# Kernel tuning notes

Hardware: AMD Instinct MI355X
Metric: run time of the kernel (lower is better)

## Reference

```python
import jax, jax.numpy as jnp
import numpy as np

C = 256; CM = 8; MAXI = 100; NCLS = 80
KP = (CM + 2) * CM + CM + CM * CM + CM + CM + 1  # 169 dynamic-kernel params

def _ln(x, g, b, eps=1e-5):
    m = x.mean(-1, keepdims=True)
    v = ((x - m) ** 2).mean(-1, keepdims=True)
    return g * (x - m) * jax.lax.rsqrt(v + eps) + b

def _mlp(x, hw, hb, lng, lnb, fw, fb):
    # torchvision MLP: [Linear -> LayerNorm -> SiLU] * n_hidden -> Linear
    for i in range(hw.shape[0]):
        x = jax.nn.silu(_ln(x @ hw[i] + hb[i], lng[i], lnb[i]))
    return x @ fw + fb

def _conv1x1_bn(x, w, s, b):
    # 1x1 conv (no bias) + inference-mode BatchNorm folded into per-channel affine
    y = jnp.einsum('bchw,oc->bohw', x, w)
    return y * s[None, :, None, None] + b[None, :, None, None]

def _grid(h, w):
    # normalized cell-center coordinates, (x, y) order, shape [h, w, 2]
    ys = (jnp.arange(h, dtype=jnp.float32) + 0.5) / h
    xs = (jnp.arange(w, dtype=jnp.float32) + 0.5) / w
    return jnp.stack([jnp.broadcast_to(xs[None, :], (h, w)),
                      jnp.broadcast_to(ys[:, None], (h, w))], axis=-1)

def setup_inputs() -> dict:
    key = jax.random.key(0)
    ks = iter(jax.random.split(key, 40))
    nrm = lambda shape, s=0.02: s * jax.random.normal(next(ks), shape, jnp.float32)
    B = 4
    inp = {
        'x0': jax.random.normal(next(ks), (B, 3, 512, 512), jnp.float32),
        'x1': jax.random.normal(next(ks), (B, 64, 256, 256), jnp.float32),
        'x2': jax.random.normal(next(ks), (B, 128, 128, 128), jnp.float32),
        'x3': jax.random.normal(next(ks), (B, 256, 64, 64), jnp.float32),
        'x4': jax.random.normal(next(ks), (B, 512, 32, 32), jnp.float32),
        'x5': jax.random.normal(next(ks), (B, 1024, 16, 16), jnp.float32),
        'lat3_w': nrm((C, 256)), 'lat3_s': jnp.ones((C,)), 'lat3_b': jnp.zeros((C,)),
        'lat4_w': nrm((C, 512)), 'lat4_s': jnp.ones((C,)), 'lat4_b': jnp.zeros((C,)),
        'lat5_w': nrm((C, 1024)), 'lat5_s': jnp.ones((C,)), 'lat5_b': jnp.zeros((C,)),
        'mlat_w': nrm((C, 256)), 'mlat_s': jnp.ones((C,)), 'mlat_b': jnp.zeros((C,)),
        'mhead_w': nrm((CM, C, 3, 3)), 'mhead_s': jnp.ones((CM,)), 'mhead_b': jnp.zeros((CM,)),
        'loc_hw': nrm((4, C, C)), 'loc_hb': jnp.zeros((4, C)), 'loc_lng': jnp.ones((4, C)), 'loc_lnb': jnp.zeros((4, C)),
        'loc_fw': nrm((C, 1)), 'loc_fb': -5.0 * jnp.ones((1,)),
        'cls_hw': nrm((4, C, C)), 'cls_hb': jnp.zeros((4, C)), 'cls_lng': jnp.ones((4, C)), 'cls_lnb': jnp.zeros((4, C)),
        'cls_fw': nrm((C, NCLS)), 'cls_fb': jnp.zeros((NCLS,)),
        'ker_hw': nrm((4, C, C)), 'ker_hb': jnp.zeros((4, C)), 'ker_lng': jnp.ones((4, C)), 'ker_lnb': jnp.zeros((4, C)),
        'ker_fw': nrm((C, KP)), 'ker_fb': jnp.zeros((KP,)),
    }
    return inp

def reference(x0, x1, x2, x3, x4, x5,
              lat3_w, lat3_s, lat3_b, lat4_w, lat4_s, lat4_b, lat5_w, lat5_s, lat5_b,
              mlat_w, mlat_s, mlat_b, mhead_w, mhead_s, mhead_b,
              loc_hw, loc_hb, loc_lng, loc_lnb, loc_fw, loc_fb,
              cls_hw, cls_hb, cls_lng, cls_lnb, cls_fw, cls_fb,
              ker_hw, ker_hb, ker_lng, ker_lnb, ker_fw, ker_fb):
    B, _, H, W = x0.shape
    lvls = [(x3, lat3_w, lat3_s, lat3_b), (x4, lat4_w, lat4_s, lat4_b), (x5, lat5_w, lat5_s, lat5_b)]
    feats = [_conv1x1_bn(x, w, s, b) for (x, w, s, b) in lvls]
    flat = jnp.concatenate([f.reshape(B, C, -1).transpose(0, 2, 1) for f in feats], axis=1)  # [B, L, C]
    loc_logits = _mlp(flat, loc_hw, loc_hb, loc_lng, loc_lnb, loc_fw, loc_fb)[..., 0]       # [B, L]
    top_vals, top_idx = jax.lax.top_k(loc_logits, MAXI)
    scores = jax.nn.sigmoid(top_vals)
    num_instances = (scores > 0.5).sum(axis=1)
    gfeat = jnp.take_along_axis(flat, top_idx[:, :, None], axis=1)  # [B, I, C]
    # mask branch
    mf = _conv1x1_bn(x3, mlat_w, mlat_s, mlat_b)
    mf = jax.lax.conv_general_dilated(mf, mhead_w, (1, 1), 'SAME', dimension_numbers=('NCHW', 'OIHW', 'NCHW'))
    mf = jax.nn.silu(mf * mhead_s[None, :, None, None] + mhead_b[None, :, None, None])  # [B, CM, h3, w3]
    h3, w3 = x3.shape[2], x3.shape[3]
    offs_flat = jnp.concatenate([_grid(x.shape[2], x.shape[3]).reshape(-1, 2) for x in (x3, x4, x5)], axis=0)
    offs = offs_flat[top_idx]                                # [B, I, 2]
    grid = _grid(h3, w3).transpose(2, 0, 1)                  # [2, h3, w3]
    grid = grid[None, None] - offs[:, :, :, None, None]      # [B, I, 2, h, w]
    mfi = jnp.broadcast_to(mf[:, None], (B, MAXI, CM, h3, w3))
    feats_i = jnp.concatenate([mfi, grid], axis=2)           # [B, I, CM+2, h, w]
    dyn = _mlp(gfeat, ker_hw, ker_hb, ker_lng, ker_lnb, ker_fw, ker_fb)  # [B, I, KP]
    c = CM
    o = (c + 2) * c
    w1 = dyn[..., :o].reshape(B, MAXI, c + 2, c)
    b1 = dyn[..., o:o + c].reshape(B, MAXI, c, 1, 1); o += c
    w2 = dyn[..., o:o + c * c].reshape(B, MAXI, c, c); o += c * c
    b2 = dyn[..., o:o + c].reshape(B, MAXI, c, 1, 1); o += c
    w3 = dyn[..., o:o + c].reshape(B, MAXI, c, 1); o += c
    b3 = dyn[..., o:].reshape(B, MAXI, 1, 1, 1)
    m = jax.nn.silu(jnp.einsum('bichw,bicd->bidhw', feats_i, w1) + b1)
    m = jax.nn.silu(jnp.einsum('bichw,bicd->bidhw', m, w2) + b2)
    m = jnp.einsum('bichw,bicd->bidhw', m, w3) + b3
    masks = jax.nn.sigmoid(m[:, :, 0])                       # [B, I, h3, w3]
    classes = jnp.argmax(_mlp(gfeat, cls_hw, cls_hb, cls_lng, cls_lnb, cls_fw, cls_fb), axis=-1)
    masks = jax.image.resize(masks, (B, MAXI, H, W), method='bilinear', antialias=False)
    return (num_instances, scores, classes, masks)
```

## Files before the change

kernel.cpp:

```cpp
#include <hip/hip_runtime.h>
#include <hip/hip_bf16.h>
#include <math.h>

#define DEVI __device__ __forceinline__

constexpr int LTOT  = 5376;
constexpr int NINST = 100;
constexpr int NCLS  = 80;
constexpr int KPAR  = 169;

DEVI float waveAllSum(float v) {
#pragma unroll
  for (int s = 32; s > 0; s >>= 1) v += __shfl_xor(v, s, 64);
  return v;
}
DEVI float siluf(float x) { return x / (1.0f + expf(-x)); }
DEVI float sigmf(float x) { return 1.0f / (1.0f + expf(-x)); }

template<int MODE>
__global__ __launch_bounds__(256) void mlp_layer(
    const float* __restrict__ in, float* __restrict__ out,
    const float* __restrict__ w0, const float* __restrict__ hb0,
    const float* __restrict__ g0, const float* __restrict__ lb0,
    const float* __restrict__ w1, const float* __restrict__ hb1,
    const float* __restrict__ g1, const float* __restrict__ lb1,
    const float* __restrict__ fw, const float* __restrict__ fb,
    float* __restrict__ logits, int rowDelta)
{
  __shared__ float xs[256][20];
  __shared__ float wsm[32][256];
  const int tid = threadIdx.x;
  const int rg = tid >> 6, cg = tid & 63;
  const long r0 = (long)blockIdx.x * 16;
  bool set1 = false;
  const float *w = w0, *hb = hb0, *g = g0, *lb = lb0;
  if (MODE == 2) {
    set1 = (blockIdx.x >= (gridDim.x >> 1));
    if (set1) { w = w1; hb = hb1; g = g1; lb = lb1; }
  }
  const long ir0 = r0 + ((MODE == 2 && set1) ? rowDelta : 0);
  {
    const int i = tid >> 4, kq = tid & 15;
    const float4* src = reinterpret_cast<const float4*>(in + (ir0 + i) * 256);
#pragma unroll
    for (int qq = 0; qq < 4; ++qq) {
      const int k4 = kq + 16 * qq;
      const float4 v = src[k4];
      xs[4*k4+0][i] = v.x; xs[4*k4+1][i] = v.y;
      xs[4*k4+2][i] = v.z; xs[4*k4+3][i] = v.w;
    }
  }
  float acc[4][4] = {};
  for (int kb = 0; kb < 8; ++kb) {
    __syncthreads();
    {
      const float4* w4 = reinterpret_cast<const float4*>(w + kb*32*256);
#pragma unroll
      for (int qb = 0; qb < 8; ++qb) {
        const int c = tid + 256*qb;
        const float4 f = w4[c];
        *reinterpret_cast<float4*>(&wsm[c>>6][4*(c&63)]) = f;
      }
    }
    __syncthreads();
#pragma unroll
    for (int kk = 0; kk < 32; ++kk) {
      const float4 wv = *reinterpret_cast<const float4*>(&wsm[kk][4*cg]);
      const float4 av = *reinterpret_cast<const float4*>(&xs[kb*32+kk][4*rg]);
      const float ar[4] = {av.x, av.y, av.z, av.w};
#pragma unroll
      for (int i = 0; i < 4; ++i) {
        acc[i][0] += ar[i]*wv.x; acc[i][1] += ar[i]*wv.y;
        acc[i][2] += ar[i]*wv.z; acc[i][3] += ar[i]*wv.w;
      }
    }
  }
  const float4 hb4 = *reinterpret_cast<const float4*>(&hb[4*cg]);
  const float4 g4  = *reinterpret_cast<const float4*>(&g[4*cg]);
  const float4 lb4 = *reinterpret_cast<const float4*>(&lb[4*cg]);
  float4 fw4 = {0,0,0,0}; float fbv = 0.f;
  if (MODE == 1) { fw4 = *reinterpret_cast<const float4*>(&fw[4*cg]); fbv = fb[0]; }
#pragma unroll
  for (int i = 0; i < 4; ++i) {
    float y0 = acc[i][0]+hb4.x, y1 = acc[i][1]+hb4.y;
    float y2 = acc[i][2]+hb4.z, y3 = acc[i][3]+hb4.w;
    const float m = waveAllSum(y0+y1+y2+y3) * (1.0f/256.0f);
    const float d0=y0-m, d1=y1-m, d2=y2-m, d3=y3-m;
    const float var = waveAllSum(d0*d0+d1*d1+d2*d2+d3*d3) * (1.0f/256.0f);
    const float rs = rsqrtf(var + 1e-5f);
    const float4 ov = { siluf(g4.x*d0*rs + lb4.x), siluf(g4.y*d1*rs + lb4.y),
                        siluf(g4.z*d2*rs + lb4.z), siluf(g4.w*d3*rs + lb4.w) };
    if (MODE == 1) {
      float dot = ov.x*fw4.x + ov.y*fw4.y + ov.z*fw4.z + ov.w*fw4.w;
      dot = waveAllSum(dot);
      if (cg == 0) logits[r0 + 4*rg + i] = dot + fbv;
    } else {
      *reinterpret_cast<float4*>(&out[(r0 + 4*rg + i)*256 + 4*cg]) = ov;
    }
  }
}

__global__ __launch_bounds__(256) void lateral_all(
    const float* __restrict__ x3, const float* __restrict__ x4, const float* __restrict__ x5,
    const float* __restrict__ w3, const float* __restrict__ s3, const float* __restrict__ b3,
    const float* __restrict__ w4, const float* __restrict__ s4, const float* __restrict__ b4,
    const float* __restrict__ w5, const float* __restrict__ s5, const float* __restrict__ b5,
    const float* __restrict__ wm, const float* __restrict__ sm, const float* __restrict__ bm,
    float* __restrict__ flat, float* __restrict__ mlatb)
{
  __shared__ float xs[32][20];
  __shared__ float wsm[32][256];
  const int tid = threadIdx.x;
  const int rg = tid >> 6, cg = tid & 63;
  const int bid = blockIdx.x;
  const float *x, *w, *sc, *bi; int K, P, pshift, rel, baseL; bool trans = true;
  if (bid < 1024)      { rel=bid;      x=x3; w=w3; sc=s3; bi=b3; K=256;  P=4096; pshift=8; baseL=0; }
  else if (bid < 1280) { rel=bid-1024; x=x4; w=w4; sc=s4; bi=b4; K=512;  P=1024; pshift=6; baseL=4096; }
  else if (bid < 1344) { rel=bid-1280; x=x5; w=w5; sc=s5; bi=b5; K=1024; P=256;  pshift=4; baseL=5120; }
  else                 { rel=bid-1344; x=x3; w=wm; sc=sm; bi=bm; K=256;  P=4096; pshift=8; baseL=0; trans=false; }
  const int b = rel >> pshift;
  const int p0 = (rel - (b << pshift)) << 4;
  const float* xb = x + (long)b * K * P;
  float acc[4][4] = {};
  const int nkb = K >> 5;
  for (int kb = 0; kb < nkb; ++kb) {
    __syncthreads();
    {
      const int kk = tid >> 4, i = tid & 15;
      xs[kk][i]    = xb[(long)(kb*32 + kk)*P + p0 + i];
      xs[kk+16][i] = xb[(long)(kb*32 + kk + 16)*P + p0 + i];
    }
    {
      const float4* wr = reinterpret_cast<const float4*>(w + (long)tid*K + kb*32);
#pragma unroll
      for (int kq = 0; kq < 8; ++kq) {
        const float4 v = wr[kq];
        wsm[4*kq+0][tid]=v.x; wsm[4*kq+1][tid]=v.y;
        wsm[4*kq+2][tid]=v.z; wsm[4*kq+3][tid]=v.w;
      }
    }
    __syncthreads();
#pragma unroll
    for (int kk = 0; kk < 32; ++kk) {
      const float4 wv = *reinterpret_cast<const float4*>(&wsm[kk][4*cg]);
      const float4 av = *reinterpret_cast<const float4*>(&xs[kk][4*rg]);
      const float ar[4] = {av.x, av.y, av.z, av.w};
#pragma unroll
      for (int i = 0; i < 4; ++i) {
        acc[i][0]+=ar[i]*wv.x; acc[i][1]+=ar[i]*wv.y;
        acc[i][2]+=ar[i]*wv.z; acc[i][3]+=ar[i]*wv.w;
      }
    }
  }
  const float4 s4v = *reinterpret_cast<const float4*>(&sc[4*cg]);
  const float4 b4v = *reinterpret_cast<const float4*>(&bi[4*cg]);
  if (trans) {
#pragma unroll
    for (int i = 0; i < 4; ++i) {
      const float4 ov = { acc[i][0]*s4v.x+b4v.x, acc[i][1]*s4v.y+b4v.y,
                          acc[i][2]*s4v.z+b4v.z, acc[i][3]*s4v.w+b4v.w };
      *reinterpret_cast<float4*>(&flat[((long)b*LTOT + baseL + p0 + 4*rg + i)*256 + 4*cg]) = ov;
    }
  } else {
    const float ss[4] = {s4v.x, s4v.y, s4v.z, s4v.w};
    const float bb[4] = {b4v.x, b4v.y, b4v.z, b4v.w};
#pragma unroll
    for (int j = 0; j < 4; ++j) {
      const float4 ov = { acc[0][j]*ss[j]+bb[j], acc[1][j]*ss[j]+bb[j],
                          acc[2][j]*ss[j]+bb[j], acc[3][j]*ss[j]+bb[j] };
      *reinterpret_cast<float4*>(&mlatb[((long)b*256 + 4*cg + j)*(long)P + p0 + 4*rg]) = ov;
    }
  }
}

__global__ __launch_bounds__(256) void topk_gather(
    const float* __restrict__ logits, const float* __restrict__ flat,
    int* __restrict__ topi, float* __restrict__ gfeat,
    float* __restrict__ dout)
{
  __shared__ float sv[LTOT];
  __shared__ float rv[4];
  __shared__ int   ri[4];
  __shared__ int   sidx[NINST];
  const int b = blockIdx.x, tid = threadIdx.x;
  for (int l = tid; l < LTOT; l += 256) sv[l] = logits[b*LTOT + l];
  __syncthreads();
  int cnt = 0;
  for (int t = 0; t < NINST; ++t) {
    float bv = -INFINITY; int bidx = 0x7fffffff;
    for (int l = tid; l < LTOT; l += 256) {
      const float v = sv[l];
      if (v > bv) { bv = v; bidx = l; }
    }
#pragma unroll
    for (int s = 32; s > 0; s >>= 1) {
      const float v2 = __shfl_xor(bv, s, 64);
      const int   i2 = __shfl_xor(bidx, s, 64);
      if (v2 > bv || (v2 == bv && i2 < bidx)) { bv = v2; bidx = i2; }
    }
    if ((tid & 63) == 0) { rv[tid >> 6] = bv; ri[tid >> 6] = bidx; }
    __syncthreads();
    if (tid == 0) {
      bv = rv[0]; bidx = ri[0];
#pragma unroll
      for (int q = 1; q < 4; ++q)
        if (rv[q] > bv || (rv[q] == bv && ri[q] < bidx)) { bv = rv[q]; bidx = ri[q]; }
      sidx[t] = bidx; topi[b*NINST + t] = bidx;
      dout[4 + b*NINST + t] = sigmf(bv);
      if (bv > 0.0f) ++cnt;
      sv[bidx] = -INFINITY;
    }
    __syncthreads();
  }
  if (tid == 0) dout[b] = (float)cnt;
  for (int t = 0; t < NINST; ++t) {
    const int ix = sidx[t];
    gfeat[((long)b*NINST + t)*256 + tid] = flat[((long)b*LTOT + ix)*256 + tid];
  }
}

__global__ __launch_bounds__(256) void heads(
    const float* __restrict__ h2, const float* __restrict__ cfw, const float* __restrict__ cfb,
    const float* __restrict__ kfw, const float* __restrict__ kfb,
    float* __restrict__ dout, float* __restrict__ dyn)
{
  __shared__ float xr[256];
  __shared__ float lv[NCLS];
  const int bid = blockIdx.x, tid = threadIdx.x;
  xr[tid] = h2[(long)bid*256 + tid];
  __syncthreads();
  if (bid < 400) {
    if (tid < NCLS) {
      float a0=0.f, a1=0.f, a2=0.f, a3=0.f;
      for (int k = 0; k < 256; k += 4) {
        a0 += xr[k+0]*cfw[(k+0)*NCLS + tid];
        a1 += xr[k+1]*cfw[(k+1)*NCLS + tid];
        a2 += xr[k+2]*cfw[(k+2)*NCLS + tid];
        a3 += xr[k+3]*cfw[(k+3)*NCLS + tid];
      }
      lv[tid] = (a0+a1) + (a2+a3) + cfb[tid];
    }
    __syncthreads();
    if (tid == 0) {
      float bv = lv[0]; int bi2 = 0;
      for (int o = 1; o < NCLS; ++o) if (lv[o] > bv) { bv = lv[o]; bi2 = o; }
      dout[404 + bid] = (float)bi2;
    }
  } else {
    if (tid < KPAR) {
      float a0=0.f, a1=0.f, a2=0.f, a3=0.f;
      for (int k = 0; k < 256; k += 4) {
        a0 += xr[k+0]*kfw[(k+0)*KPAR + tid];
        a1 += xr[k+1]*kfw[(k+1)*KPAR + tid];
        a2 += xr[k+2]*kfw[(k+2)*KPAR + tid];
        a3 += xr[k+3]*kfw[(k+3)*KPAR + tid];
      }
      dyn[(long)(bid-400)*KPAR + tid] = (a0+a1) + (a2+a3) + kfb[tid];
    }
  }
}

__global__ __launch_bounds__(256) void conv3(
    const float* __restrict__ mlat, const float* __restrict__ mw,
    float* __restrict__ partial)
{
  const int bid = blockIdx.x;
  const int cc = bid & 7;
  const int tile = (bid >> 3) & 15;
  const int b = bid >> 7;
  const int y0 = (tile >> 2)*16, x0 = (tile & 3)*16;
  const int tid = threadIdx.x;
  const int ly = tid >> 4, lx = tid & 15;
  __shared__ float til[2][18][19];
  __shared__ float wch[8][32][12];
  for (int e = tid; e < 2304; e += 256) {
    const int o = e / 288, rem = e % 288;
    const int c = rem / 9, qq = rem - c*9;
    wch[o][c][qq] = mw[((o*256) + cc*32 + c)*9 + qq];
  }
  int lofs[3], gofs[3], chn[3]; bool vld[3], has[3];
  float* tf = &til[0][0][0];
#pragma unroll
  for (int s = 0; s < 3; ++s) {
    const int e = tid + 256*s;
    has[s] = (e < 648);
    lofs[s] = 0; gofs[s] = 0; chn[s] = 0; vld[s] = false;
    if (has[s]) {
      const int ch = (e >= 324) ? 1 : 0;
      const int pos = e - ch*324;
      const int iy = pos / 18, ix = pos - iy*18;
      const int gy = y0 - 1 + iy, gx = x0 - 1 + ix;
      vld[s] = (gy >= 0 && gy < 64 && gx >= 0 && gx < 64);
      lofs[s] = ch*342 + iy*19 + ix;
      gofs[s] = gy*64 + gx;
      chn[s] = ch;
    }
  }
  const float* xbase = mlat + ((long)b*256 + cc*32)*4096;
  float acc[8] = {};
  for (int r = 0; r < 16; ++r) {
    __syncthreads();
#pragma unroll
    for (int s = 0; s < 3; ++s)
      if (has[s]) tf[lofs[s]] = vld[s] ? xbase[(long)(2*r + chn[s])*4096 + gofs[s]] : 0.f;
    __syncthreads();
#pragma unroll
    for (int ch = 0; ch < 2; ++ch) {
      const int c = 2*r + ch;
      float t[9];
#pragma unroll
      for (int dy = 0; dy < 3; ++dy)
#pragma unroll
        for (int dx = 0; dx < 3; ++dx) t[dy*3+dx] = til[ch][ly+dy][lx+dx];
#pragma unroll
      for (int o = 0; o < 8; ++o) {
        const float4 wa = *reinterpret_cast<const float4*>(&wch[o][c][0]);
        const float4 wb = *reinterpret_cast<const float4*>(&wch[o][c][4]);
        const float w8 = wch[o][c][8];
        acc[o] += t[0]*wa.x + t[1]*wa.y + t[2]*wa.z + t[3]*wa.w
                + t[4]*wb.x + t[5]*wb.y + t[6]*wb.z + t[7]*wb.w + t[8]*w8;
      }
    }
  }
  const long pbase = (((long)b*8 + cc)*8)*4096 + (y0+ly)*64 + (x0+lx);
#pragma unroll
  for (int o = 0; o < 8; ++o) partial[pbase + (long)o*4096] = acc[o];
}

__global__ __launch_bounds__(256) void mhead_fin(
    const float* __restrict__ partial, const float* __restrict__ s,
    const float* __restrict__ bi, float* __restrict__ mhead)
{
  const int idx = blockIdx.x*256 + threadIdx.x;
  const int p = idx & 4095;
  const int o = (idx >> 12) & 7;
  const int b = idx >> 15;
  float v = 0.f;
#pragma unroll
  for (int cc = 0; cc < 8; ++cc) v += partial[(((long)b*8 + cc)*8 + o)*4096 + p];
  v = v*s[o] + bi[o];
  mhead[idx] = siluf(v);
}

__global__ __launch_bounds__(256) void mask_fused(
    const float* __restrict__ dyn, const int* __restrict__ topi,
    const float* __restrict__ mhead, float* __restrict__ dout)
{
  __shared__ float msrc[18][64];
  __shared__ float dd[KPAR];
  __shared__ float so[2];
  const int bid = blockIdx.x;
  const int inst = bid >> 2, q = bid & 3;
  const int tid = threadIdx.x;
  if (tid < KPAR) dd[tid] = dyn[(long)inst*KPAR + tid];
  if (tid == 0) {
    const int l = topi[inst];
    float ox, oy;
    if (l < 4096)      { ox = ((l & 63) + 0.5f)*(1.f/64.f); oy = ((l >> 6) + 0.5f)*(1.f/64.f); }
    else if (l < 5120) { const int t = l - 4096; ox = ((t & 31) + 0.5f)*(1.f/32.f); oy = ((t >> 5) + 0.5f)*(1.f/32.f); }
    else               { const int t = l - 5120; ox = ((t & 15) + 0.5f)*(1.f/16.f); oy = ((t >> 4) + 0.5f)*(1.f/16.f); }
    so[0] = ox; so[1] = oy;
  }
  __syncthreads();
  const float ox = so[0], oy = so[1];
  const int b = inst / NINST;
  const float* mh = mhead + (long)b*8*4096;
  const int r0s = 16*q - 1;
  for (int e = tid; e < 1152; e += 256) {
    const int r = e >> 6, x = e & 63;
    int sy = r0s + r; sy = sy < 0 ? 0 : (sy > 63 ? 63 : sy);
    const int p = sy*64 + x;
    float f[10];
#pragma unroll
    for (int c = 0; c < 8; ++c) f[c] = mh[c*4096 + p];
    f[8] = (x + 0.5f)*(1.f/64.f) - ox;
    f[9] = (sy + 0.5f)*(1.f/64.f) - oy;
    float m1[8];
#pragma unroll
    for (int d = 0; d < 8; ++d) {
      float t = dd[80 + d];
#pragma unroll
      for (int c = 0; c < 10; ++c) t += f[c]*dd[c*8 + d];
      m1[d] = siluf(t);
    }
    float m2[8];
#pragma unroll
    for (int d = 0; d < 8; ++d) {
      float t = dd[152 + d];
#pragma unroll
      for (int c = 0; c < 8; ++c) t += m1[c]*dd[88 + c*8 + d];
      m2[d] = siluf(t);
    }
    float o = dd[168];
#pragma unroll
    for (int c = 0; c < 8; ++c) o += m2[c]*dd[160 + c];
    msrc[r][x] = sigmf(o);
  }
  __syncthreads();
  const int j4 = tid & 127;
  const int half = tid >> 7;
  const int ix0 = (j4 & 1) ? (j4 >> 1) : (j4 >> 1) - 1;
  const int xlo = ix0 < 0 ? 0 : ix0;
  const int xhi = (ix0 + 1 > 63) ? 63 : ix0 + 1;
  float fx[4];
#pragma unroll
  for (int m = 0; m < 4; ++m) {
    const int x = 4*j4 + m;
    const float tx = (x + 0.5f)*0.125f - 0.5f;
    fx[m] = tx - (float)ix0;
  }
  float* dbase = dout + 804 + ((long)inst << 18);
  for (int it = 0; it < 64; ++it) {
    const int yy = 2*it + half;
    const int y = 128*q + yy;
    const float ty = (y + 0.5f)*0.125f - 0.5f;
    const float fyf = floorf(ty);
    const int iy0 = (int)fyf;
    const float fy = ty - fyf;
    const int r0 = iy0 - r0s;
    const float L0 = msrc[r0][xlo],   R0 = msrc[r0][xhi];
    const float L1 = msrc[r0+1][xlo], R1 = msrc[r0+1][xhi];
    const float L = L0 + (L1 - L0)*fy;
    const float R = R0 + (R1 - R0)*fy;
    const float4 ov = { L + (R - L)*fx[0], L + (R - L)*fx[1],
                        L + (R - L)*fx[2], L + (R - L)*fx[3] };
    *reinterpret_cast<float4*>(&dbase[((long)y << 9) + (j4 << 2)]) = ov;
  }
}

extern "C" void kernel_launch(void* const* d_in, const int* in_sizes, int n_in,
                              void* d_out, int out_size, void* d_ws, size_t ws_size,
                              hipStream_t stream)
{
  (void)in_sizes; (void)n_in; (void)out_size; (void)ws_size;
  const float* x3      = (const float*)d_in[3];
  const float* x4      = (const float*)d_in[4];
  const float* x5      = (const float*)d_in[5];
  const float* lat3_w  = (const float*)d_in[6];
  const float* lat3_s  = (const float*)d_in[7];
  const float* lat3_b  = (const float*)d_in[8];
  const float* lat4_w  = (const float*)d_in[9];
  const float* lat4_s  = (const float*)d_in[10];
  const float* lat4_b  = (const float*)d_in[11];
  const float* lat5_w  = (const float*)d_in[12];
  const float* lat5_s  = (const float*)d_in[13];
  const float* lat5_b  = (const float*)d_in[14];
  const float* mlat_w  = (const float*)d_in[15];
  const float* mlat_s  = (const float*)d_in[16];
  const float* mlat_b  = (const float*)d_in[17];
  const float* mhead_w = (const float*)d_in[18];
  const float* mhead_s = (const float*)d_in[19];
  const float* mhead_b = (const float*)d_in[20];
  const float* loc_hw  = (const float*)d_in[21];
  const float* loc_hb  = (const float*)d_in[22];
  const float* loc_lng = (const float*)d_in[23];
  const float* loc_lnb = (const float*)d_in[24];
  const float* loc_fw  = (const float*)d_in[25];
  const float* loc_fb  = (const float*)d_in[26];
  const float* cls_hw  = (const float*)d_in[27];
  const float* cls_hb  = (const float*)d_in[28];
  const float* cls_lng = (const float*)d_in[29];
  const float* cls_lnb = (const float*)d_in[30];
  const float* cls_fw  = (const float*)d_in[31];
  const float* cls_fb  = (const float*)d_in[32];
  const float* ker_hw  = (const float*)d_in[33];
  const float* ker_hb  = (const float*)d_in[34];
  const float* ker_lng = (const float*)d_in[35];
  const float* ker_lnb = (const float*)d_in[36];
  const float* ker_fw  = (const float*)d_in[37];
  const float* ker_fb  = (const float*)d_in[38];

  float* ws      = (float*)d_ws;
  float* flat    = ws;
  float* buf     = ws + 5505024;
  float* mlatb   = ws + 11010048;
  float* partial = ws + 15204352;
  float* mheadb  = ws + 16252928;
  float* h2      = ws + 16384000;
  float* logits  = ws + 16588800;
  int*   topi    = (int*)(ws + 16610304);
  float* gfeat   = ws + 16610704;
  float* dynb    = ws + 16713104;
  float* dout    = (float*)d_out;

  lateral_all<<<2368, 256, 0, stream>>>(x3, x4, x5,
      lat3_w, lat3_s, lat3_b, lat4_w, lat4_s, lat4_b, lat5_w, lat5_s, lat5_b,
      mlat_w, mlat_s, mlat_b, flat, mlatb);
  conv3<<<512, 256, 0, stream>>>(mlatb, mhead_w, partial);
  mhead_fin<<<512, 256, 0, stream>>>(partial, mhead_s, mhead_b, mheadb);
  mlp_layer<0><<<1344, 256, 0, stream>>>(flat, buf,
      loc_hw, loc_hb, loc_lng, loc_lnb, nullptr, nullptr, nullptr, nullptr,
      nullptr, nullptr, nullptr, 0);
  for (int i = 1; i < 3; ++i)
    mlp_layer<0><<<1344, 256, 0, stream>>>(buf, buf,
        loc_hw + i*65536, loc_hb + i*256, loc_lng + i*256, loc_lnb + i*256,
        nullptr, nullptr, nullptr, nullptr, nullptr, nullptr, nullptr, 0);
  mlp_layer<1><<<1344, 256, 0, stream>>>(buf, nullptr,
      loc_hw + 3*65536, loc_hb + 3*256, loc_lng + 3*256, loc_lnb + 3*256,
      nullptr, nullptr, nullptr, nullptr, loc_fw, loc_fb, logits, 0);
  topk_gather<<<4, 256, 0, stream>>>(logits, flat, topi, gfeat, dout);
  mlp_layer<2><<<50, 256, 0, stream>>>(gfeat, h2,
      cls_hw, cls_hb, cls_lng, cls_lnb, ker_hw, ker_hb, ker_lng, ker_lnb,
      nullptr, nullptr, nullptr, -400);
  for (int i = 1; i < 4; ++i)
    mlp_layer<2><<<50, 256, 0, stream>>>(h2, h2,
        cls_hw + i*65536, cls_hb + i*256, cls_lng + i*256, cls_lnb + i*256,
        ker_hw + i*65536, ker_hb + i*256, ker_lng + i*256, ker_lnb + i*256,
        nullptr, nullptr, nullptr, 0);
  heads<<<800, 256, 0, stream>>>(h2, cls_fw, cls_fb, ker_fw, ker_fb, dout, dynb);
  mask_fused<<<1600, 256, 0, stream>>>(dynb, topi, mheadb, dout);
}
```

Before: 864.1 us.

## Fuse MLP layers into single kernels and merge lateral/mask-lateral GEMMs

```diff
diff --git a/kernel.cpp b/kernel.cpp
--- a/kernel.cpp
+++ b/kernel.cpp
@@ -16,89 +16,6 @@
 }
 DEVI float siluf(float x) { return x / (1.0f + expf(-x)); }
 DEVI float sigmf(float x) { return 1.0f / (1.0f + expf(-x)); }
-
-template<int MODE>
-__global__ __launch_bounds__(256) void mlp_layer(
-    const float* __restrict__ in, float* __restrict__ out,
-    const float* __restrict__ w0, const float* __restrict__ hb0,
-    const float* __restrict__ g0, const float* __restrict__ lb0,
-    const float* __restrict__ w1, const float* __restrict__ hb1,
-    const float* __restrict__ g1, const float* __restrict__ lb1,
-    const float* __restrict__ fw, const float* __restrict__ fb,
-    float* __restrict__ logits, int rowDelta)
-{
-  __shared__ float xs[256][20];
-  __shared__ float wsm[32][256];
-  const int tid = threadIdx.x;
-  const int rg = tid >> 6, cg = tid & 63;
-  const long r0 = (long)blockIdx.x * 16;
-  bool set1 = false;
-  const float *w = w0, *hb = hb0, *g = g0, *lb = lb0;
-  if (MODE == 2) {
-    set1 = (blockIdx.x >= (gridDim.x >> 1));
-    if (set1) { w = w1; hb = hb1; g = g1; lb = lb1; }
-  }
-  const long ir0 = r0 + ((MODE == 2 && set1) ? rowDelta : 0);
-  {
-    const int i = tid >> 4, kq = tid & 15;
-    const float4* src = reinterpret_cast<const float4*>(in + (ir0 + i) * 256);
-#pragma unroll
-    for (int qq = 0; qq < 4; ++qq) {
-      const int k4 = kq + 16 * qq;
-      const float4 v = src[k4];
-      xs[4*k4+0][i] = v.x; xs[4*k4+1][i] = v.y;
-      xs[4*k4+2][i] = v.z; xs[4*k4+3][i] = v.w;
-    }
-  }
-  float acc[4][4] = {};
-  for (int kb = 0; kb < 8; ++kb) {
-    __syncthreads();
-    {
-      const float4* w4 = reinterpret_cast<const float4*>(w + kb*32*256);
-#pragma unroll
-      for (int qb = 0; qb < 8; ++qb) {
-        const int c = tid + 256*qb;
-        const float4 f = w4[c];
-        *reinterpret_cast<float4*>(&wsm[c>>6][4*(c&63)]) = f;
-      }
-    }
-    __syncthreads();
-#pragma unroll
-    for (int kk = 0; kk < 32; ++kk) {
-      const float4 wv = *reinterpret_cast<const float4*>(&wsm[kk][4*cg]);
-      const float4 av = *reinterpret_cast<const float4*>(&xs[kb*32+kk][4*rg]);
-      const float ar[4] = {av.x, av.y, av.z, av.w};
-#pragma unroll
-      for (int i = 0; i < 4; ++i) {
-        acc[i][0] += ar[i]*wv.x; acc[i][1] += ar[i]*wv.y;
-        acc[i][2] += ar[i]*wv.z; acc[i][3] += ar[i]*wv.w;
-      }
-    }
-  }
-  const float4 hb4 = *reinterpret_cast<const float4*>(&hb[4*cg]);
-  const float4 g4  = *reinterpret_cast<const float4*>(&g[4*cg]);
-  const float4 lb4 = *reinterpret_cast<const float4*>(&lb[4*cg]);
-  float4 fw4 = {0,0,0,0}; float fbv = 0.f;
-  if (MODE == 1) { fw4 = *reinterpret_cast<const float4*>(&fw[4*cg]); fbv = fb[0]; }
-#pragma unroll
-  for (int i = 0; i < 4; ++i) {
-    float y0 = acc[i][0]+hb4.x, y1 = acc[i][1]+hb4.y;
-    float y2 = acc[i][2]+hb4.z, y3 = acc[i][3]+hb4.w;
-    const float m = waveAllSum(y0+y1+y2+y3) * (1.0f/256.0f);
-    const float d0=y0-m, d1=y1-m, d2=y2-m, d3=y3-m;
-    const float var = waveAllSum(d0*d0+d1*d1+d2*d2+d3*d3) * (1.0f/256.0f);
-    const float rs = rsqrtf(var + 1e-5f);
-    const float4 ov = { siluf(g4.x*d0*rs + lb4.x), siluf(g4.y*d1*rs + lb4.y),
-                        siluf(g4.z*d2*rs + lb4.z), siluf(g4.w*d3*rs + lb4.w) };
-    if (MODE == 1) {
-      float dot = ov.x*fw4.x + ov.y*fw4.y + ov.z*fw4.z + ov.w*fw4.w;
-      dot = waveAllSum(dot);
-      if (cg == 0) logits[r0 + 4*rg + i] = dot + fbv;
-    } else {
-      *reinterpret_cast<float4*>(&out[(r0 + 4*rg + i)*256 + 4*cg]) = ov;
-    }
-  }
-}
 
 __global__ __launch_bounds__(256) void lateral_all(
     const float* __restrict__ x3, const float* __restrict__ x4, const float* __restrict__ x5,
@@ -108,68 +25,175 @@
     const float* __restrict__ wm, const float* __restrict__ sm, const float* __restrict__ bm,
     float* __restrict__ flat, float* __restrict__ mlatb)
 {
-  __shared__ float xs[32][20];
-  __shared__ float wsm[32][256];
+  __shared__ float xs[16][36];
+  __shared__ float wsA[16][256];
+  __shared__ float wsB[16][256];
   const int tid = threadIdx.x;
   const int rg = tid >> 6, cg = tid & 63;
   const int bid = blockIdx.x;
-  const float *x, *w, *sc, *bi; int K, P, pshift, rel, baseL; bool trans = true;
-  if (bid < 1024)      { rel=bid;      x=x3; w=w3; sc=s3; bi=b3; K=256;  P=4096; pshift=8; baseL=0; }
-  else if (bid < 1280) { rel=bid-1024; x=x4; w=w4; sc=s4; bi=b4; K=512;  P=1024; pshift=6; baseL=4096; }
-  else if (bid < 1344) { rel=bid-1280; x=x5; w=w5; sc=s5; bi=b5; K=1024; P=256;  pshift=4; baseL=5120; }
-  else                 { rel=bid-1344; x=x3; w=wm; sc=sm; bi=bm; K=256;  P=4096; pshift=8; baseL=0; trans=false; }
-  const int b = rel >> pshift;
-  const int p0 = (rel - (b << pshift)) << 4;
+  const float *x, *wA, *wB = nullptr, *scA, *biA;
+  int K, P, b, p0, baseL; bool merged = false;
+  if (bid < 512)      { merged = true; b = bid >> 7; p0 = (bid & 127) * 32;
+                        x = x3; wA = w3; wB = wm; scA = s3; biA = b3; K = 256; P = 4096; baseL = 0; }
+  else if (bid < 640) { const int rel = bid - 512; b = rel >> 5; p0 = (rel & 31) * 32;
+                        x = x4; wA = w4; scA = s4; biA = b4; K = 512; P = 1024; baseL = 4096; }
+  else                { const int rel = bid - 640; b = rel >> 3; p0 = (rel & 7) * 32;
+                        x = x5; wA = w5; scA = s5; biA = b5; K = 1024; P = 256; baseL = 5120; }
   const float* xb = x + (long)b * K * P;
-  float acc[4][4] = {};
-  const int nkb = K >> 5;
+  float accA[8][4] = {};
+  float accB[8][4] = {};
+  const int nkb = K >> 4;
   for (int kb = 0; kb < nkb; ++kb) {
     __syncthreads();
+#pragma unroll
+    for (int s = 0; s < 2; ++s) {
+      const int e = tid + 256*s;
+      const int kk = e >> 5, px = e & 31;
+      xs[kk][px] = xb[(kb*16 + kk)*P + p0 + px];
+    }
     {
-      const int kk = tid >> 4, i = tid & 15;
-      xs[kk][i]    = xb[(long)(kb*32 + kk)*P + p0 + i];
-      xs[kk+16][i] = xb[(long)(kb*32 + kk + 16)*P + p0 + i];
-    }
-    {
-      const float4* wr = reinterpret_cast<const float4*>(w + (long)tid*K + kb*32);
-#pragma unroll
-      for (int kq = 0; kq < 8; ++kq) {
-        const float4 v = wr[kq];
-        wsm[4*kq+0][tid]=v.x; wsm[4*kq+1][tid]=v.y;
-        wsm[4*kq+2][tid]=v.z; wsm[4*kq+3][tid]=v.w;
-      }
-    }
-    __syncthreads();
-#pragma unroll
-    for (int kk = 0; kk < 32; ++kk) {
-      const float4 wv = *reinterpret_cast<const float4*>(&wsm[kk][4*cg]);
-      const float4 av = *reinterpret_cast<const float4*>(&xs[kk][4*rg]);
-      const float ar[4] = {av.x, av.y, av.z, av.w};
-#pragma unroll
-      for (int i = 0; i < 4; ++i) {
-        acc[i][0]+=ar[i]*wv.x; acc[i][1]+=ar[i]*wv.y;
-        acc[i][2]+=ar[i]*wv.z; acc[i][3]+=ar[i]*wv.w;
-      }
-    }
-  }
-  const float4 s4v = *reinterpret_cast<const float4*>(&sc[4*cg]);
-  const float4 b4v = *reinterpret_cast<const float4*>(&bi[4*cg]);
-  if (trans) {
-#pragma unroll
-    for (int i = 0; i < 4; ++i) {
-      const float4 ov = { acc[i][0]*s4v.x+b4v.x, acc[i][1]*s4v.y+b4v.y,
-                          acc[i][2]*s4v.z+b4v.z, acc[i][3]*s4v.w+b4v.w };
-      *reinterpret_cast<float4*>(&flat[((long)b*LTOT + baseL + p0 + 4*rg + i)*256 + 4*cg]) = ov;
-    }
-  } else {
-    const float ss[4] = {s4v.x, s4v.y, s4v.z, s4v.w};
-    const float bb[4] = {b4v.x, b4v.y, b4v.z, b4v.w};
+      const float4* wr = reinterpret_cast<const float4*>(wA + (long)tid*K + kb*16);
+#pragma unroll
+      for (int q = 0; q < 4; ++q) {
+        const float4 v = wr[q];
+        wsA[4*q+0][tid]=v.x; wsA[4*q+1][tid]=v.y; wsA[4*q+2][tid]=v.z; wsA[4*q+3][tid]=v.w;
+      }
+      if (merged) {
+        const float4* wr2 = reinterpret_cast<const float4*>(wB + (long)tid*K + kb*16);
+#pragma unroll
+        for (int q = 0; q < 4; ++q) {
+          const float4 v = wr2[q];
+          wsB[4*q+0][tid]=v.x; wsB[4*q+1][tid]=v.y; wsB[4*q+2][tid]=v.z; wsB[4*q+3][tid]=v.w;
+        }
+      }
+    }
+    __syncthreads();
+#pragma unroll
+    for (int kk = 0; kk < 16; ++kk) {
+      const float4 a0 = *reinterpret_cast<const float4*>(&xs[kk][8*rg]);
+      const float4 a1 = *reinterpret_cast<const float4*>(&xs[kk][8*rg+4]);
+      const float ar[8] = {a0.x,a0.y,a0.z,a0.w,a1.x,a1.y,a1.z,a1.w};
+      const float4 wv = *reinterpret_cast<const float4*>(&wsA[kk][4*cg]);
+#pragma unroll
+      for (int i = 0; i < 8; ++i) {
+        accA[i][0] += ar[i]*wv.x; accA[i][1] += ar[i]*wv.y;
+        accA[i][2] += ar[i]*wv.z; accA[i][3] += ar[i]*wv.w;
+      }
+      if (merged) {
+        const float4 wv2 = *reinterpret_cast<const float4*>(&wsB[kk][4*cg]);
+#pragma unroll
+        for (int i = 0; i < 8; ++i) {
+          accB[i][0] += ar[i]*wv2.x; accB[i][1] += ar[i]*wv2.y;
+          accB[i][2] += ar[i]*wv2.z; accB[i][3] += ar[i]*wv2.w;
+        }
+      }
+    }
+  }
+  const float4 sA = *reinterpret_cast<const float4*>(&scA[4*cg]);
+  const float4 bA = *reinterpret_cast<const float4*>(&biA[4*cg]);
+#pragma unroll
+  for (int i = 0; i < 8; ++i) {
+    const float4 ov = { accA[i][0]*sA.x+bA.x, accA[i][1]*sA.y+bA.y,
+                        accA[i][2]*sA.z+bA.z, accA[i][3]*sA.w+bA.w };
+    *reinterpret_cast<float4*>(&flat[((long)b*LTOT + baseL + p0 + 8*rg + i)*256 + 4*cg]) = ov;
+  }
+  if (merged) {
+    const float4 sB = *reinterpret_cast<const float4*>(&sm[4*cg]);
+    const float4 bB = *reinterpret_cast<const float4*>(&bm[4*cg]);
 #pragma unroll
     for (int j = 0; j < 4; ++j) {
-      const float4 ov = { acc[0][j]*ss[j]+bb[j], acc[1][j]*ss[j]+bb[j],
-                          acc[2][j]*ss[j]+bb[j], acc[3][j]*ss[j]+bb[j] };
-      *reinterpret_cast<float4*>(&mlatb[((long)b*256 + 4*cg + j)*(long)P + p0 + 4*rg]) = ov;
-    }
+      const float sj = (&sB.x)[j], bj = (&bB.x)[j];
+      const float4 o0 = { accB[0][j]*sj+bj, accB[1][j]*sj+bj, accB[2][j]*sj+bj, accB[3][j]*sj+bj };
+      const float4 o1 = { accB[4][j]*sj+bj, accB[5][j]*sj+bj, accB[6][j]*sj+bj, accB[7][j]*sj+bj };
+      float* mb = &mlatb[((long)b*256 + 4*cg + j)*4096 + p0 + 8*rg];
+      *reinterpret_cast<float4*>(mb) = o0;
+      *reinterpret_cast<float4*>(mb + 4) = o1;
+    }
+  }
+}
+
+__global__ __launch_bounds__(256) void loc4(
+    const float* __restrict__ in, const float* __restrict__ hw,
+    const float* __restrict__ hb, const float* __restrict__ lng, const float* __restrict__ lnb,
+    const float* __restrict__ fw, const float* __restrict__ fb, float* __restrict__ logits)
+{
+  __shared__ float xs[256][36];
+  __shared__ float wsm[16][256];
+  const int tid = threadIdx.x;
+  const int rg = tid >> 6, cg = tid & 63;
+  const long r0 = (long)blockIdx.x * 32;
+#pragma unroll
+  for (int s = 0; s < 8; ++s) {
+    const int e = tid + 256*s;
+    const int row = e >> 6, q = e & 63;
+    const float4 v = *reinterpret_cast<const float4*>(&in[(r0 + row)*256 + 4*q]);
+    const int pc = 8*((row >> 3) ^ (q & 3)) + (row & 7);
+#pragma unroll
+    for (int j = 0; j < 4; ++j) xs[4*q+j][pc] = (&v.x)[j];
+  }
+  float ov[8][4];
+  for (int L = 0; L < 4; ++L) {
+    const float* w = hw + L*65536;
+    float acc[8][4] = {};
+    for (int kb = 0; kb < 16; ++kb) {
+      __syncthreads();
+      const float4* w4 = reinterpret_cast<const float4*>(w + (kb << 12));
+#pragma unroll
+      for (int q = 0; q < 4; ++q) {
+        const int c = tid + (q << 8);
+        *reinterpret_cast<float4*>(&wsm[c>>6][4*(c&63)]) = w4[c];
+      }
+      __syncthreads();
+#pragma unroll
+      for (int kk = 0; kk < 16; ++kk) {
+        const int k = (kb << 4) + kk;
+        const int col = 8*(rg ^ ((k >> 2) & 3));
+        const float4 a0 = *reinterpret_cast<const float4*>(&xs[k][col]);
+        const float4 a1 = *reinterpret_cast<const float4*>(&xs[k][col+4]);
+        const float4 wv = *reinterpret_cast<const float4*>(&wsm[kk][4*cg]);
+        const float ar[8] = {a0.x,a0.y,a0.z,a0.w,a1.x,a1.y,a1.z,a1.w};
+#pragma unroll
+        for (int i = 0; i < 8; ++i) {
+          acc[i][0] += ar[i]*wv.x; acc[i][1] += ar[i]*wv.y;
+          acc[i][2] += ar[i]*wv.z; acc[i][3] += ar[i]*wv.w;
+        }
+      }
+    }
+    const float4 hb4 = *reinterpret_cast<const float4*>(&hb[L*256 + 4*cg]);
+    const float4 g4  = *reinterpret_cast<const float4*>(&lng[L*256 + 4*cg]);
+    const float4 lb4 = *reinterpret_cast<const float4*>(&lnb[L*256 + 4*cg]);
+#pragma unroll
+    for (int i = 0; i < 8; ++i) {
+      const float y0 = acc[i][0]+hb4.x, y1 = acc[i][1]+hb4.y;
+      const float y2 = acc[i][2]+hb4.z, y3 = acc[i][3]+hb4.w;
+      const float m = waveAllSum(y0+y1+y2+y3) * (1.0f/256.0f);
+      const float d0=y0-m, d1=y1-m, d2=y2-m, d3=y3-m;
+      const float var = waveAllSum(d0*d0+d1*d1+d2*d2+d3*d3) * (1.0f/256.0f);
+      const float rs = rsqrtf(var + 1e-5f);
+      ov[i][0] = siluf(g4.x*d0*rs + lb4.x);
+      ov[i][1] = siluf(g4.y*d1*rs + lb4.y);
+      ov[i][2] = siluf(g4.z*d2*rs + lb4.z);
+      ov[i][3] = siluf(g4.w*d3*rs + lb4.w);
+    }
+    __syncthreads();
+    if (L < 3) {
+      const int colb = 8*(rg ^ (cg & 3));
+#pragma unroll
+      for (int j = 0; j < 4; ++j) {
+        const float4 t0 = {ov[0][j], ov[1][j], ov[2][j], ov[3][j]};
+        const float4 t1 = {ov[4][j], ov[5][j], ov[6][j], ov[7][j]};
+        *reinterpret_cast<float4*>(&xs[4*cg+j][colb])   = t0;
+        *reinterpret_cast<float4*>(&xs[4*cg+j][colb+4]) = t1;
+      }
+    }
+  }
+  const float4 fw4 = *reinterpret_cast<const float4*>(&fw[4*cg]);
+  const float fbv = fb[0];
+#pragma unroll
+  for (int i = 0; i < 8; ++i) {
+    float d = ov[i][0]*fw4.x + ov[i][1]*fw4.y + ov[i][2]*fw4.z + ov[i][3]*fw4.w;
+    d = waveAllSum(d);
+    if (cg == 0) logits[r0 + 8*rg + i] = d + fbv;
   }
 }
 
@@ -216,6 +240,88 @@
   for (int t = 0; t < NINST; ++t) {
     const int ix = sidx[t];
     gfeat[((long)b*NINST + t)*256 + tid] = flat[((long)b*LTOT + ix)*256 + tid];
+  }
+}
+
+__global__ __launch_bounds__(256) void clsker4(
+    const float* __restrict__ gfeat, float* __restrict__ h2,
+    const float* __restrict__ chw, const float* __restrict__ chb,
+    const float* __restrict__ cg_, const float* __restrict__ cb_,
+    const float* __restrict__ khw, const float* __restrict__ khb,
+    const float* __restrict__ kg_, const float* __restrict__ kb_)
+{
+  __shared__ float xs[256][12];
+  __shared__ float wsm[16][256];
+  const int tid = threadIdx.x;
+  const int rg = tid >> 6, cg = tid & 63;
+  const bool ker = blockIdx.x >= 50;
+  const int r0 = (ker ? (blockIdx.x - 50) : blockIdx.x) * 8;
+  const int outr0 = r0 + (ker ? 400 : 0);
+  const float* hw = ker ? khw : chw;
+  const float* hb = ker ? khb : chb;
+  const float* g_ = ker ? kg_ : cg_;
+  const float* lb = ker ? kb_ : cb_;
+#pragma unroll
+  for (int s = 0; s < 2; ++s) {
+    const int e = tid + 256*s;
+    const int row = e >> 6, q = e & 63;
+    const float4 v = *reinterpret_cast<const float4*>(&gfeat[(long)(r0 + row)*256 + 4*q]);
+    const int pc = 2*((row >> 1) ^ (q & 3)) + (row & 1);
+#pragma unroll
+    for (int j = 0; j < 4; ++j) xs[4*q+j][pc] = (&v.x)[j];
+  }
+  float ov[2][4];
+  for (int L = 0; L < 4; ++L) {
+    const float* w = hw + L*65536;
+    float acc[2][4] = {};
+    for (int kb = 0; kb < 16; ++kb) {
+      __syncthreads();
+      const float4* w4 = reinterpret_cast<const float4*>(w + (kb << 12));
+#pragma unroll
+      for (int q = 0; q < 4; ++q) {
+        const int c = tid + (q << 8);
+        *reinterpret_cast<float4*>(&wsm[c>>6][4*(c&63)]) = w4[c];
+      }
+      __syncthreads();
+#pragma unroll
+      for (int kk = 0; kk < 16; ++kk) {
+        const int k = (kb << 4) + kk;
+        const float2 av = *reinterpret_cast<const float2*>(&xs[k][2*(rg ^ ((k >> 2) & 3))]);
+        const float4 wv = *reinterpret_cast<const float4*>(&wsm[kk][4*cg]);
+        acc[0][0] += av.x*wv.x; acc[0][1] += av.x*wv.y; acc[0][2] += av.x*wv.z; acc[0][3] += av.x*wv.w;
+        acc[1][0] += av.y*wv.x; acc[1][1] += av.y*wv.y; acc[1][2] += av.y*wv.z; acc[1][3] += av.y*wv.w;
+      }
+    }
+    const float4 hb4 = *reinterpret_cast<const float4*>(&hb[L*256 + 4*cg]);
+    const float4 g4  = *reinterpret_cast<const float4*>(&g_[L*256 + 4*cg]);
+    const float4 lb4 = *reinterpret_cast<const float4*>(&lb[L*256 + 4*cg]);
+#pragma unroll
+    for (int i = 0; i < 2; ++i) {
+      const float y0 = acc[i][0]+hb4.x, y1 = acc[i][1]+hb4.y;
+      const float y2 = acc[i][2]+hb4.z, y3 = acc[i][3]+hb4.w;
+      const float m = waveAllSum(y0+y1+y2+y3) * (1.0f/256.0f);
+      const float d0=y0-m, d1=y1-m, d2=y2-m, d3=y3-m;
+      const float var = waveAllSum(d0*d0+d1*d1+d2*d2+d3*d3) * (1.0f/256.0f);
+      const float rs = rsqrtf(var + 1e-5f);
+      ov[i][0] = siluf(g4.x*d0*rs + lb4.x);
+      ov[i][1] = siluf(g4.y*d1*rs + lb4.y);
+      ov[i][2] = siluf(g4.z*d2*rs + lb4.z);
+      ov[i][3] = siluf(g4.w*d3*rs + lb4.w);
+    }
+    __syncthreads();
+    if (L < 3) {
+      const int pc = 2*(rg ^ (cg & 3));
+#pragma unroll
+      for (int j = 0; j < 4; ++j) {
+        const float2 t = {ov[0][j], ov[1][j]};
+        *reinterpret_cast<float2*>(&xs[4*cg+j][pc]) = t;
+      }
+    }
+  }
+#pragma unroll
+  for (int i = 0; i < 2; ++i) {
+    const float4 o = {ov[i][0], ov[i][1], ov[i][2], ov[i][3]};
+    *reinterpret_cast<float4*>(&h2[(long)(outr0 + 2*rg + i)*256 + 4*cg]) = o;
   }
 }
 
@@ -373,8 +479,8 @@
     float f[10];
 #pragma unroll
     for (int c = 0; c < 8; ++c) f[c] = mh[c*4096 + p];
-    f[8] = (x + 0.5f)*(1.f/64.f) - ox;
-    f[9] = (sy + 0.5f)*(1.f/64.f) - oy;
+    f[8] = ((x) + 0.5f)*(1.f/64.f) - ox;
+    f[9] = ((sy) + 0.5f)*(1.f/64.f) - oy;
     float m1[8];
 #pragma unroll
     for (int d = 0; d < 8; ++d) {
@@ -422,9 +528,9 @@
     const float L1 = msrc[r0+1][xlo], R1 = msrc[r0+1][xhi];
     const float L = L0 + (L1 - L0)*fy;
     const float R = R0 + (R1 - R0)*fy;
-    const float4 ov = { L + (R - L)*fx[0], L + (R - L)*fx[1],
-                        L + (R - L)*fx[2], L + (R - L)*fx[3] };
-    *reinterpret_cast<float4*>(&dbase[((long)y << 9) + (j4 << 2)]) = ov;
+    const float4 ovv = { L + (R - L)*fx[0], L + (R - L)*fx[1],
+                         L + (R - L)*fx[2], L + (R - L)*fx[3] };
+    *reinterpret_cast<float4*>(&dbase[((long)y << 9) + (j4 << 2)]) = ovv;
   }
 }
 
@@ -472,41 +578,26 @@
 
   float* ws      = (float*)d_ws;
   float* flat    = ws;
-  float* buf     = ws + 5505024;
-  float* mlatb   = ws + 11010048;
-  float* partial = ws + 15204352;
-  float* mheadb  = ws + 16252928;
-  float* h2      = ws + 16384000;
-  float* logits  = ws + 16588800;
-  int*   topi    = (int*)(ws + 16610304);
-  float* gfeat   = ws + 16610704;
-  float* dynb    = ws + 16713104;
+  float* mlatb   = ws + 5505024;
+  float* partial = ws + 9699328;
+  float* mheadb  = ws + 10747904;
+  float* h2      = ws + 10878976;
+  float* logits  = ws + 11083776;
+  int*   topi    = (int*)(ws + 11105280);
+  float* gfeat   = ws + 11105680;
+  float* dynb    = ws + 11208080;
   float* dout    = (float*)d_out;
 
-  lateral_all<<<2368, 256, 0, stream>>>(x3, x4, x5,
+  lateral_all<<<672, 256, 0, stream>>>(x3, x4, x5,
       lat3_w, lat3_s, lat3_b, lat4_w, lat4_s, lat4_b, lat5_w, lat5_s, lat5_b,
       mlat_w, mlat_s, mlat_b, flat, mlatb);
   conv3<<<512, 256, 0, stream>>>(mlatb, mhead_w, partial);
   mhead_fin<<<512, 256, 0, stream>>>(partial, mhead_s, mhead_b, mheadb);
-  mlp_layer<0><<<1344, 256, 0, stream>>>(flat, buf,
-      loc_hw, loc_hb, loc_lng, loc_lnb, nullptr, nullptr, nullptr, nullptr,
-      nullptr, nullptr, nullptr, 0);
-  for (int i = 1; i < 3; ++i)
-    mlp_layer<0><<<1344, 256, 0, stream>>>(buf, buf,
-        loc_hw + i*65536, loc_hb + i*256, loc_lng + i*256, loc_lnb + i*256,
-        nullptr, nullptr, nullptr, nullptr, nullptr, nullptr, nullptr, 0);
-  mlp_layer<1><<<1344, 256, 0, stream>>>(buf, nullptr,
-      loc_hw + 3*65536, loc_hb + 3*256, loc_lng + 3*256, loc_lnb + 3*256,
-      nullptr, nullptr, nullptr, nullptr, loc_fw, loc_fb, logits, 0);
+  loc4<<<672, 256, 0, stream>>>(flat, loc_hw, loc_hb, loc_lng, loc_lnb,
+                                loc_fw, loc_fb, logits);
   topk_gather<<<4, 256, 0, stream>>>(logits, flat, topi, gfeat, dout);
-  mlp_layer<2><<<50, 256, 0, stream>>>(gfeat, h2,
-      cls_hw, cls_hb, cls_lng, cls_lnb, ker_hw, ker_hb, ker_lng, ker_lnb,
-      nullptr, nullptr, nullptr, -400);
-  for (int i = 1; i < 4; ++i)
-    mlp_layer<2><<<50, 256, 0, stream>>>(h2, h2,
-        cls_hw + i*65536, cls_hb + i*256, cls_lng + i*256, cls_lnb + i*256,
-        ker_hw + i*65536, ker_hb + i*256, ker_lng + i*256, ker_lnb + i*256,
-        nullptr, nullptr, nullptr, 0);
+  clsker4<<<100, 256, 0, stream>>>(gfeat, h2,
+      cls_hw, cls_hb, cls_lng, cls_lnb, ker_hw, ker_hb, ker_lng, ker_lnb);
   heads<<<800, 256, 0, stream>>>(h2, cls_fw, cls_fb, ker_fw, ker_fb, dout, dynb);
   mask_fused<<<1600, 256, 0, stream>>>(dynb, topi, mheadb, dout);
 }
```

After: 1.155 ms. 1.34x slower.
